# Optimization experiments

Hardware: AMD Instinct MI355X
Metric: run time of the kernel (lower is better)

## Reference

```python
import jax, jax.numpy as jnp
import numpy as np

N_NODES = 500000
N_EDGES = 4000000
K = 4  # TAGConv hops


def _gcn_norm(edge_index, edge_weight, num_nodes):
    # PyG gcn_norm with add_self_loops=False (TAGConv default)
    src, dst = edge_index[0], edge_index[1]
    deg = jax.ops.segment_sum(edge_weight, dst, num_segments=num_nodes)
    dinv = jnp.where(deg > 0, jax.lax.rsqrt(deg), 0.0)
    return dinv[src] * edge_weight * dinv[dst]


def _tag_conv(x, src, dst, norm, Ws, b, num_nodes):
    # out = sum_{k=0..K} x_k @ Ws[k] + b,  x_k = hat(A) x_{k-1}
    out = x @ Ws[0]
    h = x
    for k in range(1, K + 1):
        msg = norm[:, None] * h[src]                      # [E, C]
        h = jax.ops.segment_sum(msg, dst, num_segments=num_nodes)
        out = out + h @ Ws[k]
    return out + b


def setup_inputs() -> dict:
    key = jax.random.key(0)
    ks = jax.random.split(key, 8)
    x = jax.random.normal(ks[0], (N_NODES, 2), dtype=jnp.float32)
    edge_index = jax.random.randint(ks[1], (2, N_EDGES), 0, N_NODES, dtype=jnp.int64)
    edge_weight = jax.random.uniform(ks[2], (N_EDGES,), dtype=jnp.float32)
    W1 = jax.random.normal(ks[3], (K + 1, 2, 16), dtype=jnp.float32) * 0.4
    b1 = jax.random.normal(ks[4], (16,), dtype=jnp.float32) * 0.1
    W2 = jax.random.normal(ks[5], (K + 1, 16, 16), dtype=jnp.float32) * 0.15
    b2 = jax.random.normal(ks[6], (16,), dtype=jnp.float32) * 0.1
    Wend = jax.random.normal(ks[7], (16, 1), dtype=jnp.float32) * 0.25
    return {"x": x, "edge_index": edge_index, "edge_weight": edge_weight,
            "W1": W1, "b1": b1, "W2": W2, "b2": b2, "Wend": Wend}


def reference(x, edge_index, edge_weight, W1, b1, W2, b2, Wend):
    src, dst = edge_index[0], edge_index[1]
    norm = _gcn_norm(edge_index, edge_weight, N_NODES)
    h = _tag_conv(x, src, dst, norm, W1, b1, N_NODES)      # conv1: 2 -> 16
    # num_layers=3 -> one relu+conv2 iteration
    h = jax.nn.relu(h)
    h = _tag_conv(h, src, dst, norm, W2, b2, N_NODES)      # conv2: 16 -> 16
    h = jax.nn.relu(h)
    y = h @ Wend                                           # endLinear (no bias)
    return jax.nn.sigmoid(y)                               # [N, 1]
```

## Files before the change

kernel.cpp:

```cpp
#include <hip/hip_runtime.h>
#include <hip/hip_fp16.h>
#include <math.h>


#define TB 256
#define TBIN 1024
#define BSHIFT 9
#define BW 512
#define CAP 4608
#define BIN_CHUNK 16384
#define WQ 8191.0f

__global__ __launch_bounds__(TBIN) void bin_kernel(
        const int* __restrict__ src, const int* __restrict__ dst,
        const float* __restrict__ w, int* __restrict__ binCount,
        uint2* __restrict__ binBuf, int E, int NB) {
    __shared__ int bcnt[1024];
    __shared__ int bbase[1024];
    for (int i = threadIdx.x; i < 1024; i += TBIN) bcnt[i] = 0;
    __syncthreads();

    int base = blockIdx.x * BIN_CHUNK;
    int d[16];
#pragma unroll
    for (int j = 0; j < 16; j++) {
        int e = base + threadIdx.x + j * TBIN;
        d[j] = (e < E) ? dst[e] : -1;
        if (d[j] >= 0) atomicAdd(&bcnt[d[j] >> BSHIFT], 1);
    }
    __syncthreads();
    for (int i = threadIdx.x; i < NB; i += TBIN) {
        int c = bcnt[i];
        bbase[i] = c ? atomicAdd(&binCount[i], c) : 0;
        bcnt[i] = 0;
    }
    __syncthreads();
#pragma unroll
    for (int j = 0; j < 16; j++) {
        if (d[j] >= 0) {
            int e = base + threadIdx.x + j * TBIN;
            int b = d[j] >> BSHIFT;
            int off = bbase[b] + atomicAdd(&bcnt[b], 1);
            if (off < CAP) {
                binBuf[(size_t)b * CAP + off] =
                    make_uint2((unsigned)src[e] | ((unsigned)(d[j] & (BW - 1)) << 20),
                               __float_as_uint(w[e]));
            }
        }
    }
}

__global__ void build_kernel(const int* __restrict__ binCount, const uint2* __restrict__ binBuf,
                             unsigned* __restrict__ payload, int* __restrict__ seg,
                             float* __restrict__ dinv2, float* __restrict__ rdinv,
                             const float* __restrict__ x, __half2* __restrict__ z0,
                             int N, int NB) {
    __shared__ int   cnt[BW];
    __shared__ float wsum[BW];
    __shared__ int   start[BW];
    __shared__ int   tmp[TB];
    int b = blockIdx.x;
    int nBase = b << BSHIFT;
    int nCount = min(BW, N - nBase);
    int m = min(binCount[b], CAP);

    for (int i = threadIdx.x; i < BW; i += TB) { cnt[i] = 0; wsum[i] = 0.0f; }
    __syncthreads();

    const uint2* recs = binBuf + (size_t)b * CAP;
    for (int i = threadIdx.x; i < m; i += TB) {
        uint2 r = recs[i];
        int ld = r.x >> 20;
        atomicAdd(&cnt[ld], 1);
        atomicAdd(&wsum[ld], __uint_as_float(r.y));
    }
    __syncthreads();

    int i0 = threadIdx.x * 2;
    int c0 = cnt[i0], c1 = cnt[i0 + 1];
    int s = c0 + c1;
    tmp[threadIdx.x] = s;
    __syncthreads();
    for (int off = 1; off < TB; off <<= 1) {
        int t = (threadIdx.x >= off) ? tmp[threadIdx.x - off] : 0;
        __syncthreads();
        tmp[threadIdx.x] += t;
        __syncthreads();
    }
    int excl = tmp[threadIdx.x] - s;
    start[i0] = excl;
    start[i0 + 1] = excl + c0;
    __syncthreads();

    size_t pbase = (size_t)b * CAP;
    for (int i = threadIdx.x; i < nCount; i += TB) {
        int n = nBase + i;
        seg[n] = start[i] | (cnt[i] << 13);
        float dsum = wsum[i];
        float di = (dsum > 0.0f) ? rsqrtf(dsum) : 0.0f;
        dinv2[n] = di * di;
        rdinv[n] = dsum * di;
        float2 xv = reinterpret_cast<const float2*>(x)[n];
        z0[n] = __float22half2_rn(make_float2(di * xv.x, di * xv.y));
    }
    __syncthreads();
    for (int i = threadIdx.x; i < BW; i += TB) cnt[i] = start[i];
    __syncthreads();
    for (int i = threadIdx.x; i < m; i += TB) {
        uint2 r = recs[i];
        int ld = r.x >> 20;
        int pos = atomicAdd(&cnt[ld], 1);
        unsigned q = (unsigned)__float2int_rn(__uint_as_float(r.y) * WQ);
        payload[pbase + pos] = (r.x & 0x7FFFFu) | (q << 19);
    }
}


__device__ __forceinline__ void gacc2(const unsigned* __restrict__ payload,
                                      const __half2* __restrict__ zin,
                                      int beg, int end, float& ax, float& ay) {
    int i = beg;
    for (; i + 8 <= end; i += 8) {
        unsigned r[8];
        __half2 v[8];
#pragma unroll
        for (int j = 0; j < 8; j++) r[j] = payload[i + j];
#pragma unroll
        for (int j = 0; j < 8; j++) v[j] = zin[r[j] & 0x7FFFFu];
#pragma unroll
        for (int j = 0; j < 8; j++) {
            float wv = (float)(r[j] >> 19) * (1.0f / WQ);
            float2 f = __half22float2(v[j]);
            ax += wv * f.x;
            ay += wv * f.y;
        }
    }
    for (; i < end; i++) {
        unsigned r = payload[i];
        float wv = (float)(r >> 19) * (1.0f / WQ);
        float2 f = __half22float2(zin[r & 0x7FFFFu]);
        ax += wv * f.x;
        ay += wv * f.y;
    }
}

__device__ __forceinline__ void gacc16(const unsigned* __restrict__ payload,
                                       const __half* __restrict__ uin,
                                       int beg, int end, float* __restrict__ h) {
    int i = beg;
    for (; i + 4 <= end; i += 4) {
        unsigned r[4];
        float4 a[4], b[4];
#pragma unroll
        for (int j = 0; j < 4; j++) r[j] = payload[i + j];
#pragma unroll
        for (int j = 0; j < 4; j++) {
            const float4* up = reinterpret_cast<const float4*>(uin + 16LL * (int)(r[j] & 0x7FFFFu));
            a[j] = up[0];
            b[j] = up[1];
        }
#pragma unroll
        for (int j = 0; j < 4; j++) {
            float wv = (float)(r[j] >> 19) * (1.0f / WQ);
            const __half2* h0 = reinterpret_cast<const __half2*>(&a[j]);
            const __half2* h1 = reinterpret_cast<const __half2*>(&b[j]);
#pragma unroll
            for (int q = 0; q < 4; q++) {
                float2 v = __half22float2(h0[q]);
                h[2 * q + 0] += wv * v.x;
                h[2 * q + 1] += wv * v.y;
                float2 u = __half22float2(h1[q]);
                h[8 + 2 * q + 0] += wv * u.x;
                h[8 + 2 * q + 1] += wv * u.y;
            }
        }
    }
    for (; i < end; i++) {
        unsigned r = payload[i];
        float wv = (float)(r >> 19) * (1.0f / WQ);
        const float4* up = reinterpret_cast<const float4*>(uin + 16LL * (int)(r & 0x7FFFFu));
        float4 a = up[0], b = up[1];
        const __half2* h0 = reinterpret_cast<const __half2*>(&a);
        const __half2* h1 = reinterpret_cast<const __half2*>(&b);
#pragma unroll
        for (int q = 0; q < 4; q++) {
            float2 v = __half22float2(h0[q]);
            h[2 * q + 0] += wv * v.x;
            h[2 * q + 1] += wv * v.y;
            float2 u = __half22float2(h1[q]);
            h[8 + 2 * q + 0] += wv * u.x;
            h[8 + 2 * q + 1] += wv * u.y;
        }
    }
}


__global__ void hop2_kernel(const int* __restrict__ seg, const unsigned* __restrict__ payload,
                            const __half2* __restrict__ zin, const float* __restrict__ dinv2,
                            __half2* __restrict__ zout, int N) {
    int n = blockIdx.x * TB + threadIdx.x;
    if (n >= N) return;
    int sp = seg[n];
    int beg = (n >> BSHIFT) * CAP + (sp & 0x1FFF);
    int end = beg + (sp >> 13);
    float ax = 0.0f, ay = 0.0f;
    gacc2(payload, zin, beg, end, ax, ay);
    float sc = dinv2[n];
    zout[n] = __float22half2_rn(make_float2(ax * sc, ay * sc));
}

__global__ void hop2_final_kernel(const int* __restrict__ seg, const unsigned* __restrict__ payload,
                                  const __half2* __restrict__ zbuf,
                                  const float* __restrict__ x,
                                  const float* __restrict__ rdinv, const float* __restrict__ dinv2,
                                  const float* __restrict__ W1, const float* __restrict__ b1,
                                  __half* __restrict__ g0, __half* __restrict__ u0, int N) {
    __shared__ float Ws[160];
    __shared__ float bs[16];
    for (int i = threadIdx.x; i < 160; i += blockDim.x) Ws[i] = W1[i];
    if (threadIdx.x < 16) bs[threadIdx.x] = b1[threadIdx.x];
    __syncthreads();

    int n = blockIdx.x * TB + threadIdx.x;
    if (n >= N) return;

    int sp = seg[n];
    int beg = (n >> BSHIFT) * CAP + (sp & 0x1FFF);
    int end = beg + (sp >> 13);
    const __half2* z3 = zbuf + (size_t)3 * N;
    float ax = 0.0f, ay = 0.0f;
    gacc2(payload, z3, beg, end, ax, ay);
    float sc = dinv2[n];
    float rd = rdinv[n];

    float coeff[10];
    {
        float2 v = reinterpret_cast<const float2*>(x)[n];
        coeff[0] = v.x; coeff[1] = v.y;
    }
#pragma unroll
    for (int k = 1; k <= 3; k++) {
        float2 v = __half22float2(zbuf[(size_t)k * N + n]);
        coeff[2 * k + 0] = rd * v.x;
        coeff[2 * k + 1] = rd * v.y;
    }
    coeff[8] = rd * sc * ax;
    coeff[9] = rd * sc * ay;

    float o[16];
#pragma unroll
    for (int c = 0; c < 16; c++) o[c] = bs[c];
#pragma unroll
    for (int j = 0; j < 10; j++) {
        float cf = coeff[j];
#pragma unroll
        for (int c = 0; c < 16; c++) o[c] += cf * Ws[j * 16 + c];
    }
#pragma unroll
    for (int c = 0; c < 16; c++) o[c] = fmaxf(o[c], 0.0f);

    float di = sc * rd;

    __half2 gp[8], up[8];
#pragma unroll
    for (int q = 0; q < 8; q++) {
        gp[q] = __float22half2_rn(make_float2(o[2 * q], o[2 * q + 1]));
        up[q] = __float22half2_rn(make_float2(di * o[2 * q], di * o[2 * q + 1]));
    }
    float4* gw = reinterpret_cast<float4*>(g0 + 16LL * n);
    gw[0] = *reinterpret_cast<float4*>(&gp[0]);
    gw[1] = *reinterpret_cast<float4*>(&gp[4]);
    float4* uw = reinterpret_cast<float4*>(u0 + 16LL * n);
    uw[0] = *reinterpret_cast<float4*>(&up[0]);
    uw[1] = *reinterpret_cast<float4*>(&up[4]);
}

__global__ void hop16_kernel(const int* __restrict__ seg, const unsigned* __restrict__ payload,
                             const __half* __restrict__ uin, const float* __restrict__ dinv2,
                             __half* __restrict__ uout, int N) {
    int n = blockIdx.x * TB + threadIdx.x;
    if (n >= N) return;
    int sp = seg[n];
    int beg = (n >> BSHIFT) * CAP + (sp & 0x1FFF);
    int end = beg + (sp >> 13);

    float h[16];
#pragma unroll
    for (int c = 0; c < 16; c++) h[c] = 0.0f;
    gacc16(payload, uin, beg, end, h);

    float sc = dinv2[n];
    __half2 p[8];
#pragma unroll
    for (int q = 0; q < 8; q++)
        p[q] = __float22half2_rn(make_float2(h[2 * q] * sc, h[2 * q + 1] * sc));
    float4* uw = reinterpret_cast<float4*>(uout + 16LL * n);
    uw[0] = *reinterpret_cast<float4*>(&p[0]);
    uw[1] = *reinterpret_cast<float4*>(&p[4]);
}

__global__ void hop16_final_kernel(const int* __restrict__ seg, const unsigned* __restrict__ payload,
                                   const __half* __restrict__ g0, const __half* __restrict__ ubuf,
                                   const float* __restrict__ rdinv, const float* __restrict__ dinv2,
                                   const float* __restrict__ W2, const float* __restrict__ b2,
                                   const float* __restrict__ Wend, float* __restrict__ out, int N) {
    __shared__ float Ws[1280];
    __shared__ float bs[16];
    __shared__ float we[16];
    for (int i = threadIdx.x; i < 1280; i += blockDim.x) Ws[i] = W2[i];
    if (threadIdx.x < 16) { bs[threadIdx.x] = b2[threadIdx.x]; we[threadIdx.x] = Wend[threadIdx.x]; }
    __syncthreads();

    int n = blockIdx.x * TB + threadIdx.x;
    if (n >= N) return;

    int sp = seg[n];
    int beg = (n >> BSHIFT) * CAP + (sp & 0x1FFF);
    int end = beg + (sp >> 13);
    const __half* u3 = ubuf + (size_t)3 * 16 * N;
    float h[16];
#pragma unroll
    for (int c = 0; c < 16; c++) h[c] = 0.0f;
    gacc16(payload, u3, beg, end, h);

    float rd = rdinv[n];
    float sc = dinv2[n];

    float o[16];
#pragma unroll
    for (int c = 0; c < 16; c++) o[c] = bs[c];

    {
        const float4* gp = reinterpret_cast<const float4*>(g0 + 16LL * n);
        float4 q0 = gp[0], q1 = gp[1];
        const __half2* h0 = reinterpret_cast<const __half2*>(&q0);
        const __half2* h1 = reinterpret_cast<const __half2*>(&q1);
        float f[16];
#pragma unroll
        for (int q = 0; q < 4; q++) {
            float2 v = __half22float2(h0[q]); f[2 * q] = v.x; f[2 * q + 1] = v.y;
            float2 u = __half22float2(h1[q]); f[8 + 2 * q] = u.x; f[8 + 2 * q + 1] = u.y;
        }
#pragma unroll
        for (int j = 0; j < 16; j++) {
            float cf = f[j];
#pragma unroll
            for (int c = 0; c < 16; c++) o[c] += cf * Ws[j * 16 + c];
        }
    }

#pragma unroll
    for (int k = 1; k <= 3; k++) {
        const float4* up = reinterpret_cast<const float4*>(ubuf + (size_t)k * 16 * N + 16LL * n);
        float4 q0 = up[0], q1 = up[1];
        const __half2* h0 = reinterpret_cast<const __half2*>(&q0);
        const __half2* h1 = reinterpret_cast<const __half2*>(&q1);
        float f[16];
#pragma unroll
        for (int q = 0; q < 4; q++) {
            float2 v = __half22float2(h0[q]); f[2 * q] = v.x; f[2 * q + 1] = v.y;
            float2 u = __half22float2(h1[q]); f[8 + 2 * q] = u.x; f[8 + 2 * q + 1] = u.y;
        }
#pragma unroll
        for (int j = 0; j < 16; j++) {
            float cf = rd * f[j];
#pragma unroll
            for (int c = 0; c < 16; c++) o[c] += cf * Ws[(k * 16 + j) * 16 + c];
        }
    }

    {
        float s4 = rd * sc;
#pragma unroll
        for (int j = 0; j < 16; j++) {
            float cf = s4 * h[j];
#pragma unroll
            for (int c = 0; c < 16; c++) o[c] += cf * Ws[(4 * 16 + j) * 16 + c];
        }
    }

    float s = 0.0f;
#pragma unroll
    for (int c = 0; c < 16; c++) s += fmaxf(o[c], 0.0f) * we[c];
    out[n] = 1.0f / (1.0f + __expf(-s));
}

extern "C" void kernel_launch(void* const* d_in, const int* in_sizes, int n_in,
                              void* d_out, int out_size, void* d_ws, size_t ws_size,
                              hipStream_t stream) {
    const float* x    = (const float*)d_in[0];
    const int*   ei   = (const int*)d_in[1];
    const float* w    = (const float*)d_in[2];
    const float* W1   = (const float*)d_in[3];
    const float* b1   = (const float*)d_in[4];
    const float* W2   = (const float*)d_in[5];
    const float* b2   = (const float*)d_in[6];
    const float* Wend = (const float*)d_in[7];
    float* out = (float*)d_out;

    const int N = in_sizes[0] / 2;
    const int E = in_sizes[2];
    const int NB = (N + BW - 1) / BW;

    const int* src = ei;
    const int* dst = ei + E;

    int*      binCount = (int*)d_ws;
    unsigned* payload  = (unsigned*)(binCount + 1024);
    int*      seg      = (int*)(payload + (size_t)NB * CAP);
    float*    dinv2    = (float*)(seg + N);
    float*    rdinv    = dinv2 + N;
    __half2*  zbuf     = (__half2*)(rdinv + N);
    __half*   g0       = (__half*)(zbuf + (size_t)4 * N);
    __half*   ubuf     = g0 + (size_t)16 * N;
    uint2*    binBuf   = (uint2*)(ubuf + (size_t)16 * N);

    const int gE_bin = (E + BIN_CHUNK - 1) / BIN_CHUNK;
    const int gN = (N + TB - 1) / TB;

    hipMemsetAsync(binCount, 0, 1024 * sizeof(int), stream);

    bin_kernel<<<gE_bin, TBIN, 0, stream>>>(src, dst, w, binCount, binBuf, E, NB);
    build_kernel<<<NB, TB, 0, stream>>>(binCount, binBuf, payload, seg, dinv2, rdinv, x, zbuf, N, NB);

    for (int k = 1; k <= 3; k++) {
        hop2_kernel<<<gN, TB, 0, stream>>>(seg, payload, zbuf + (size_t)(k - 1) * N,
                                           dinv2, zbuf + (size_t)k * N, N);
    }
    hop2_final_kernel<<<gN, TB, 0, stream>>>(seg, payload, zbuf, x, rdinv, dinv2,
                                             W1, b1, g0, ubuf, N);

    for (int k = 1; k <= 3; k++) {
        hop16_kernel<<<gN, TB, 0, stream>>>(seg, payload, ubuf + (size_t)(k - 1) * 16 * N,
                                            dinv2, ubuf + (size_t)k * 16 * N, N);
    }
    hop16_final_kernel<<<gN, TB, 0, stream>>>(seg, payload, g0, ubuf, rdinv, dinv2,
                                              W2, b2, Wend, out, N);
}
```

Before: 610.2 us.

## Split 16-channel hop gathers across two threads per node

```diff
diff --git a/kernel.cpp b/kernel.cpp
--- a/kernel.cpp
+++ b/kernel.cpp
@@ -144,52 +144,32 @@
     }
 }
 
-__device__ __forceinline__ void gacc16(const unsigned* __restrict__ payload,
-                                       const __half* __restrict__ uin,
-                                       int beg, int end, float* __restrict__ h) {
-    int i = beg;
-    for (; i + 4 <= end; i += 4) {
-        unsigned r[4];
-        float4 a[4], b[4];
-#pragma unroll
-        for (int j = 0; j < 4; j++) r[j] = payload[i + j];
-#pragma unroll
-        for (int j = 0; j < 4; j++) {
-            const float4* up = reinterpret_cast<const float4*>(uin + 16LL * (int)(r[j] & 0x7FFFFu));
-            a[j] = up[0];
-            b[j] = up[1];
-        }
-#pragma unroll
-        for (int j = 0; j < 4; j++) {
-            float wv = (float)(r[j] >> 19) * (1.0f / WQ);
-            const __half2* h0 = reinterpret_cast<const __half2*>(&a[j]);
-            const __half2* h1 = reinterpret_cast<const __half2*>(&b[j]);
+__device__ __forceinline__ void gacc8(const unsigned* __restrict__ payload,
+                                      const __half* __restrict__ ubase,
+                                      int beg, int end, float* __restrict__ h) {
+    for (int i = beg; i < end; i += 8) {
+        float wv[8];
+        int idx[8];
+        float4 a[8];
+#pragma unroll
+        for (int j = 0; j < 8; j++) {
+            unsigned rr = payload[i + j];
+            bool valid = (i + j < end);
+            wv[j] = valid ? (float)(rr >> 19) * (1.0f / WQ) : 0.0f;
+            idx[j] = valid ? (int)(rr & 0x7FFFFu) : 0;
+        }
+#pragma unroll
+        for (int j = 0; j < 8; j++)
+            a[j] = *reinterpret_cast<const float4*>(ubase + 16LL * idx[j]);
+#pragma unroll
+        for (int j = 0; j < 8; j++) {
+            const __half2* hp = reinterpret_cast<const __half2*>(&a[j]);
 #pragma unroll
             for (int q = 0; q < 4; q++) {
-                float2 v = __half22float2(h0[q]);
-                h[2 * q + 0] += wv * v.x;
-                h[2 * q + 1] += wv * v.y;
-                float2 u = __half22float2(h1[q]);
-                h[8 + 2 * q + 0] += wv * u.x;
-                h[8 + 2 * q + 1] += wv * u.y;
+                float2 v = __half22float2(hp[q]);
+                h[2 * q + 0] += wv[j] * v.x;
+                h[2 * q + 1] += wv[j] * v.y;
             }
-        }
-    }
-    for (; i < end; i++) {
-        unsigned r = payload[i];
-        float wv = (float)(r >> 19) * (1.0f / WQ);
-        const float4* up = reinterpret_cast<const float4*>(uin + 16LL * (int)(r & 0x7FFFFu));
-        float4 a = up[0], b = up[1];
-        const __half2* h0 = reinterpret_cast<const __half2*>(&a);
-        const __half2* h1 = reinterpret_cast<const __half2*>(&b);
-#pragma unroll
-        for (int q = 0; q < 4; q++) {
-            float2 v = __half22float2(h0[q]);
-            h[2 * q + 0] += wv * v.x;
-            h[2 * q + 1] += wv * v.y;
-            float2 u = __half22float2(h1[q]);
-            h[8 + 2 * q + 0] += wv * u.x;
-            h[8 + 2 * q + 1] += wv * u.y;
         }
     }
 }
@@ -278,25 +258,24 @@
 __global__ void hop16_kernel(const int* __restrict__ seg, const unsigned* __restrict__ payload,
                              const __half* __restrict__ uin, const float* __restrict__ dinv2,
                              __half* __restrict__ uout, int N) {
-    int n = blockIdx.x * TB + threadIdx.x;
+    int gid = blockIdx.x * TB + threadIdx.x;
+    int n = gid >> 1, half = gid & 1;
     if (n >= N) return;
     int sp = seg[n];
     int beg = (n >> BSHIFT) * CAP + (sp & 0x1FFF);
     int end = beg + (sp >> 13);
 
-    float h[16];
-#pragma unroll
-    for (int c = 0; c < 16; c++) h[c] = 0.0f;
-    gacc16(payload, uin, beg, end, h);
+    float h[8];
+#pragma unroll
+    for (int c = 0; c < 8; c++) h[c] = 0.0f;
+    gacc8(payload, uin + 8 * half, beg, end, h);
 
     float sc = dinv2[n];
-    __half2 p[8];
-#pragma unroll
-    for (int q = 0; q < 8; q++)
+    __half2 p[4];
+#pragma unroll
+    for (int q = 0; q < 4; q++)
         p[q] = __float22half2_rn(make_float2(h[2 * q] * sc, h[2 * q + 1] * sc));
-    float4* uw = reinterpret_cast<float4*>(uout + 16LL * n);
-    uw[0] = *reinterpret_cast<float4*>(&p[0]);
-    uw[1] = *reinterpret_cast<float4*>(&p[4]);
+    *reinterpret_cast<float4*>(uout + 16LL * n + 8 * half) = *reinterpret_cast<float4*>(&p[0]);
 }
 
 __global__ void hop16_final_kernel(const int* __restrict__ seg, const unsigned* __restrict__ payload,
@@ -311,78 +290,79 @@
     if (threadIdx.x < 16) { bs[threadIdx.x] = b2[threadIdx.x]; we[threadIdx.x] = Wend[threadIdx.x]; }
     __syncthreads();
 
-    int n = blockIdx.x * TB + threadIdx.x;
+    int gid = blockIdx.x * TB + threadIdx.x;
+    int n = gid >> 1, half = gid & 1;
     if (n >= N) return;
 
     int sp = seg[n];
     int beg = (n >> BSHIFT) * CAP + (sp & 0x1FFF);
     int end = beg + (sp >> 13);
     const __half* u3 = ubuf + (size_t)3 * 16 * N;
-    float h[16];
-#pragma unroll
-    for (int c = 0; c < 16; c++) h[c] = 0.0f;
-    gacc16(payload, u3, beg, end, h);
+    float h[8];
+#pragma unroll
+    for (int c = 0; c < 8; c++) h[c] = 0.0f;
+    gacc8(payload, u3 + 8 * half, beg, end, h);
 
     float rd = rdinv[n];
     float sc = dinv2[n];
+    int jbase = 8 * half;
 
     float o[16];
 #pragma unroll
-    for (int c = 0; c < 16; c++) o[c] = bs[c];
+    for (int c = 0; c < 16; c++) o[c] = half ? 0.0f : bs[c];
 
     {
-        const float4* gp = reinterpret_cast<const float4*>(g0 + 16LL * n);
-        float4 q0 = gp[0], q1 = gp[1];
-        const __half2* h0 = reinterpret_cast<const __half2*>(&q0);
-        const __half2* h1 = reinterpret_cast<const __half2*>(&q1);
-        float f[16];
+        float4 q0 = *reinterpret_cast<const float4*>(g0 + 16LL * n + jbase);
+        const __half2* hp = reinterpret_cast<const __half2*>(&q0);
+        float f[8];
 #pragma unroll
         for (int q = 0; q < 4; q++) {
-            float2 v = __half22float2(h0[q]); f[2 * q] = v.x; f[2 * q + 1] = v.y;
-            float2 u = __half22float2(h1[q]); f[8 + 2 * q] = u.x; f[8 + 2 * q + 1] = u.y;
-        }
-#pragma unroll
-        for (int j = 0; j < 16; j++) {
-            float cf = f[j];
-#pragma unroll
-            for (int c = 0; c < 16; c++) o[c] += cf * Ws[j * 16 + c];
+            float2 v = __half22float2(hp[q]); f[2 * q] = v.x; f[2 * q + 1] = v.y;
+        }
+#pragma unroll
+        for (int jj = 0; jj < 8; jj++) {
+            float cf = f[jj];
+#pragma unroll
+            for (int c = 0; c < 16; c++) o[c] += cf * Ws[(jbase + jj) * 16 + c];
         }
     }
 
 #pragma unroll
     for (int k = 1; k <= 3; k++) {
-        const float4* up = reinterpret_cast<const float4*>(ubuf + (size_t)k * 16 * N + 16LL * n);
-        float4 q0 = up[0], q1 = up[1];
-        const __half2* h0 = reinterpret_cast<const __half2*>(&q0);
-        const __half2* h1 = reinterpret_cast<const __half2*>(&q1);
-        float f[16];
+        float4 q0 = *reinterpret_cast<const float4*>(ubuf + (size_t)k * 16 * N + 16LL * n + jbase);
+        const __half2* hp = reinterpret_cast<const __half2*>(&q0);
+        float f[8];
 #pragma unroll
         for (int q = 0; q < 4; q++) {
-            float2 v = __half22float2(h0[q]); f[2 * q] = v.x; f[2 * q + 1] = v.y;
-            float2 u = __half22float2(h1[q]); f[8 + 2 * q] = u.x; f[8 + 2 * q + 1] = u.y;
-        }
-#pragma unroll
-        for (int j = 0; j < 16; j++) {
-            float cf = rd * f[j];
-#pragma unroll
-            for (int c = 0; c < 16; c++) o[c] += cf * Ws[(k * 16 + j) * 16 + c];
+            float2 v = __half22float2(hp[q]); f[2 * q] = v.x; f[2 * q + 1] = v.y;
+        }
+#pragma unroll
+        for (int jj = 0; jj < 8; jj++) {
+            float cf = rd * f[jj];
+#pragma unroll
+            for (int c = 0; c < 16; c++) o[c] += cf * Ws[(k * 16 + jbase + jj) * 16 + c];
         }
     }
 
     {
         float s4 = rd * sc;
 #pragma unroll
-        for (int j = 0; j < 16; j++) {
-            float cf = s4 * h[j];
-#pragma unroll
-            for (int c = 0; c < 16; c++) o[c] += cf * Ws[(4 * 16 + j) * 16 + c];
-        }
-    }
-
-    float s = 0.0f;
-#pragma unroll
-    for (int c = 0; c < 16; c++) s += fmaxf(o[c], 0.0f) * we[c];
-    out[n] = 1.0f / (1.0f + __expf(-s));
+        for (int jj = 0; jj < 8; jj++) {
+            float cf = s4 * h[jj];
+#pragma unroll
+            for (int c = 0; c < 16; c++) o[c] += cf * Ws[(4 * 16 + jbase + jj) * 16 + c];
+        }
+    }
+
+#pragma unroll
+    for (int c = 0; c < 16; c++) o[c] += __shfl_xor(o[c], 1, 64);
+
+    if (half == 0) {
+        float s = 0.0f;
+#pragma unroll
+        for (int c = 0; c < 16; c++) s += fmaxf(o[c], 0.0f) * we[c];
+        out[n] = 1.0f / (1.0f + __expf(-s));
+    }
 }
 
 extern "C" void kernel_launch(void* const* d_in, const int* in_sizes, int n_in,
@@ -407,7 +387,7 @@
 
     int*      binCount = (int*)d_ws;
     unsigned* payload  = (unsigned*)(binCount + 1024);
-    int*      seg      = (int*)(payload + (size_t)NB * CAP);
+    int*      seg      = (int*)(payload + (size_t)NB * CAP + 8);
     float*    dinv2    = (float*)(seg + N);
     float*    rdinv    = dinv2 + N;
     __half2*  zbuf     = (__half2*)(rdinv + N);
@@ -416,7 +396,8 @@
     uint2*    binBuf   = (uint2*)(ubuf + (size_t)16 * N);
 
     const int gE_bin = (E + BIN_CHUNK - 1) / BIN_CHUNK;
-    const int gN = (N + TB - 1) / TB;
+    const int gN  = (N + TB - 1) / TB;
+    const int gN2 = (2 * N + TB - 1) / TB;
 
     hipMemsetAsync(binCount, 0, 1024 * sizeof(int), stream);
 
@@ -431,9 +412,9 @@
                                              W1, b1, g0, ubuf, N);
 
     for (int k = 1; k <= 3; k++) {
-        hop16_kernel<<<gN, TB, 0, stream>>>(seg, payload, ubuf + (size_t)(k - 1) * 16 * N,
-                                            dinv2, ubuf + (size_t)k * 16 * N, N);
-    }
-    hop16_final_kernel<<<gN, TB, 0, stream>>>(seg, payload, g0, ubuf, rdinv, dinv2,
-                                              W2, b2, Wend, out, N);
-}
+        hop16_kernel<<<gN2, TB, 0, stream>>>(seg, payload, ubuf + (size_t)(k - 1) * 16 * N,
+                                             dinv2, ubuf + (size_t)k * 16 * N, N);
+    }
+    hop16_final_kernel<<<gN2, TB, 0, stream>>>(seg, payload, g0, ubuf, rdinv, dinv2,
+                                               W2, b2, Wend, out, N);
+}
```

Result: faster. 586.3 us (-3.9%).
